# Kernel tuning notes

Measured on AMD Instinct MI355X. Metric: run time of the kernel, lower is better.

## Reference

```python
import jax, jax.numpy as jnp
import numpy as np

N_NODES = 50000
N_EDGES = 100000
NODE_DIM = 6
EDGE_DIM = 4
H = 64        # hidden_dim
HEADS = 4
T = 3         # n_iterations
RED = 16      # CBAM reduction ratio
Z_VALUES = np.array([7.98, 22.98, 38.98, 53.98, 89.98, 180.48], np.float32)


def _ln(x, g, b, eps=1e-5):
    mu = jnp.mean(x, -1, keepdims=True)
    v = jnp.mean((x - mu) ** 2, -1, keepdims=True)
    return (x - mu) * jax.lax.rsqrt(v + eps) * g + b


def _conv1d(x, w, b, pad):
    y = jax.lax.conv_general_dilated(x, w, (1,), [(pad, pad)],
                                     dimension_numbers=('NCH', 'OIH', 'NCH'))
    return y + b[None, :, None]


def _cbam(x, w1, b1, w2, b2, cw1, cb1, cw2, cb2):
    # channel attention: pool over node dim -> [1, 2H] -> MLP -> sigmoid
    cat = jnp.concatenate([x.max(0, keepdims=True), x.mean(0, keepdims=True)], 1)
    cw = jax.nn.sigmoid(jnp.maximum(cat @ w1 + b1, 0.0) @ w2 + b2)  # [1, H]
    x = x * cw
    # spatial attention: pool over feature dim -> conv1d stack over node axis
    sp = jnp.stack([x.max(-1), x.mean(-1)], 0)[None]                # [1, 2, N]
    s = jnp.maximum(_conv1d(sp, cw1, cb1, 2), 0.0)
    s = jax.nn.sigmoid(_conv1d(s, cw2, cb2, 1))                     # [1, 1, N]
    return x * s[0, 0][:, None]


def _forward(x, edge_attr, z_table, W_node, b_node, W_edge, b_edge,
             cn_w1, cn_b1, cn_w2, cn_b2, cn_cw1, cn_cb1, cn_cw2, cn_cb2,
             ce_w1, ce_b1, ce_w2, ce_b2, ce_cw1, ce_cb1, ce_cw2, ce_cb2,
             ln_comb_g, ln_comb_b, Wq, bq, Wk, bk, Wv, bv, Wskip, bskip,
             ln_tc_g, ln_tc_b, Wpn, bpn, Wpe, bpe, Wg, bg,
             Wc1, bc1, Wc2, bc2, edge_index, z_keys):
    n = x.shape[0]
    # bidirectional edges
    src = jnp.concatenate([edge_index[0], edge_index[1]])
    dst = jnp.concatenate([edge_index[1], edge_index[0]])
    eab = jnp.concatenate([edge_attr, edge_attr], 0)
    rel = x[src, :3] - x[dst, :3]

    # z embedding lookup (non-matching z -> index 0, matching torch default)
    zint = jnp.round(x[:, 2]).astype(jnp.int32)
    zidx = jnp.argmax(zint[:, None] == z_keys[None, :], 1)

    nf = jnp.maximum(x @ W_node + b_node, 0.0) + z_table[zidx]
    nf = _cbam(nf, cn_w1, cn_b1, cn_w2, cn_b2, cn_cw1, cn_cb1, cn_cw2, cn_cb2)
    ef = jnp.maximum(jnp.concatenate([eab, rel], 1) @ W_edge + b_edge, 0.0)
    ef = _cbam(ef, ce_w1, ce_b1, ce_w2, ce_b2, ce_cw1, ce_cb1, ce_cw2, ce_cb2)

    scale = float(1.0 / np.sqrt(H))
    for i in range(T):
        x0, e0 = nf, ef
        agg = jax.ops.segment_sum(ef, dst, num_segments=n)
        comb = _ln(jnp.concatenate([nf, agg - nf], 1), ln_comb_g[i], ln_comb_b[i])
        # TransformerConv (PyG): q at dst, k/v at src, segment softmax over dst
        q = (comb @ Wq[i] + bq[i]).reshape(n, HEADS, H)
        k = (comb @ Wk[i] + bk[i]).reshape(n, HEADS, H)
        v = (comb @ Wv[i] + bv[i]).reshape(n, HEADS, H)
        logits = jnp.sum(q[dst] * k[src], -1) * scale           # [2E, HEADS]
        m = jax.ops.segment_max(logits, dst, num_segments=n)
        p = jnp.exp(logits - m[dst])
        denom = jax.ops.segment_sum(p, dst, num_segments=n)
        alpha = p / denom[dst]
        out = jax.ops.segment_sum(alpha[..., None] * v[src], dst, num_segments=n)
        out = out.reshape(n, HEADS * H) + comb @ Wskip[i] + bskip[i]
        out = _ln(out, ln_tc_g[i], ln_tc_b[i])
        npj = out @ Wpn[i] + bpn[i]
        epj = out[src] @ Wpe[i] + bpe[i]
        g = jax.nn.sigmoid(jnp.concatenate([x0, npj], 1) @ Wg[i] + bg[i])
        nf = x0 * g + npj * (1.0 - g)
        g2 = jax.nn.sigmoid(jnp.concatenate([e0, epj], 1) @ Wg[i] + bg[i])
        ef = e0 * g2 + epj * (1.0 - g2)

    s_idx, e_idx = edge_index[0], edge_index[1]
    clf = jnp.concatenate([nf[s_idx], nf[e_idx]], 1)
    return (jnp.maximum(clf @ Wc1 + bc1, 0.0) @ Wc2 + bc2)[:, 0]


def setup_inputs() -> dict:
    key = jax.random.key(0)
    ks = iter(jax.random.split(key, 80))
    def nrm(shape, s=0.05):
        return jax.random.normal(next(ks), shape, jnp.float32) * s
    x = jax.random.normal(next(ks), (N_NODES, NODE_DIM), jnp.float32)
    zch = jax.random.randint(next(ks), (N_NODES,), 0, len(Z_VALUES))
    x = x.at[:, 2].set(jnp.asarray(Z_VALUES)[zch])
    edge_index = jax.random.randint(next(ks), (2, N_EDGES), 0, N_NODES)
    edge_attr = jax.random.normal(next(ks), (N_EDGES, EDGE_DIM), jnp.float32)
    z_keys = jnp.asarray(np.round(Z_VALUES).astype(np.int32))
    HH, r = HEADS * H, H // RED
    def zeros(*s):
        return jnp.zeros(s, jnp.float32)
    inp = dict(
        x=x, edge_attr=edge_attr, edge_index=edge_index, z_keys=z_keys,
        z_table=nrm((len(Z_VALUES), H)),
        W_node=nrm((NODE_DIM, H)), b_node=zeros(H),
        W_edge=nrm((EDGE_DIM + 3, H)), b_edge=zeros(H),
        cn_w1=nrm((2 * H, r)), cn_b1=zeros(r), cn_w2=nrm((r, H)), cn_b2=zeros(H),
        cn_cw1=nrm((1, 2, 5)), cn_cb1=zeros(1), cn_cw2=nrm((1, 1, 3)), cn_cb2=zeros(1),
        ce_w1=nrm((2 * H, r)), ce_b1=zeros(r), ce_w2=nrm((r, H)), ce_b2=zeros(H),
        ce_cw1=nrm((1, 2, 5)), ce_cb1=zeros(1), ce_cw2=nrm((1, 1, 3)), ce_cb2=zeros(1),
        ln_comb_g=jnp.ones((T, 2 * H), jnp.float32), ln_comb_b=zeros(T, 2 * H),
        Wq=nrm((T, 2 * H, HH)), bq=zeros(T, HH),
        Wk=nrm((T, 2 * H, HH)), bk=zeros(T, HH),
        Wv=nrm((T, 2 * H, HH)), bv=zeros(T, HH),
        Wskip=nrm((T, 2 * H, HH)), bskip=zeros(T, HH),
        ln_tc_g=jnp.ones((T, HH), jnp.float32), ln_tc_b=zeros(T, HH),
        Wpn=nrm((T, HH, H)), bpn=zeros(T, H),
        Wpe=nrm((T, HH, H)), bpe=zeros(T, H),
        Wg=nrm((T, 2 * H, H)), bg=zeros(T, H),
        Wc1=nrm((2 * H, H)), bc1=zeros(H), Wc2=nrm((H, 1)), bc2=zeros(1),
    )
    return inp


def reference(x, edge_attr, edge_index, z_keys, z_table, W_node, b_node, W_edge, b_edge,
              cn_w1, cn_b1, cn_w2, cn_b2, cn_cw1, cn_cb1, cn_cw2, cn_cb2,
              ce_w1, ce_b1, ce_w2, ce_b2, ce_cw1, ce_cb1, ce_cw2, ce_cb2,
              ln_comb_g, ln_comb_b, Wq, bq, Wk, bk, Wv, bv, Wskip, bskip,
              ln_tc_g, ln_tc_b, Wpn, bpn, Wpe, bpe, Wg, bg, Wc1, bc1, Wc2, bc2):
    return _forward(x, edge_attr, z_table, W_node, b_node, W_edge, b_edge,
                    cn_w1, cn_b1, cn_w2, cn_b2, cn_cw1, cn_cb1, cn_cw2, cn_cb2,
                    ce_w1, ce_b1, ce_w2, ce_b2, ce_cw1, ce_cb1, ce_cw2, ce_cb2,
                    ln_comb_g, ln_comb_b, Wq, bq, Wk, bk, Wv, bv, Wskip, bskip,
                    ln_tc_g, ln_tc_b, Wpn, bpn, Wpe, bpe, Wg, bg,
                    Wc1, bc1, Wc2, bc2, edge_index, z_keys)
```

## Files before the change

kernel.cpp:

```cpp
#include <hip/hip_runtime.h>


#define LN_EPS 1e-5f
#define PBLK 512

typedef __attribute__((ext_vector_type(8))) short bf16x8;
typedef __attribute__((ext_vector_type(4))) float f32x4;

static __device__ __forceinline__ float wsum(float v) {
#pragma unroll
  for (int d = 32; d > 0; d >>= 1) v += __shfl_xor(v, d);
  return v;
}
static __device__ __forceinline__ float sigm(float x) { return 1.0f / (1.0f + __expf(-x)); }
static __device__ __forceinline__ unsigned short f2bf(float f) {
  unsigned int u = __float_as_uint(f);
  u += 0x7FFFu + ((u >> 16) & 1u);
  return (unsigned short)(u >> 16);
}
static __device__ __forceinline__ float bf2f(unsigned short b) {
  return __uint_as_float(((unsigned int)b) << 16);
}
static __device__ __forceinline__ float4 ld4v(const float* p) { return *(const float4*)p; }
static __device__ __forceinline__ float4 ld4v(const unsigned short* p) {
  union { uint2 u; unsigned short h[4]; } t;
  t.u = *(const uint2*)p;
  return make_float4(bf2f(t.h[0]), bf2f(t.h[1]), bf2f(t.h[2]), bf2f(t.h[3]));
}
static __device__ __forceinline__ void st4v(float* p, float4 v) { *(float4*)p = v; }
static __device__ __forceinline__ void st4v(unsigned short* p, float4 v) {
  union { uint2 u; unsigned short h[4]; } t;
  t.h[0] = f2bf(v.x); t.h[1] = f2bf(v.y); t.h[2] = f2bf(v.z); t.h[3] = f2bf(v.w);
  *(uint2*)p = t.u;
}

__global__ __launch_bounds__(256) void k_zero2(int* __restrict__ a, int* __restrict__ b, int n) {
  int i = blockIdx.x * 256 + threadIdx.x;
  if (i < n) { a[i] = 0; b[i] = 0; }
}

__global__ __launch_bounds__(256) void k_sentinel(float* __restrict__ out, int n) {
  int i = blockIdx.x * 256 + threadIdx.x;
  if (i < n) out[i] = 1.0e6f;
}

__global__ __launch_bounds__(256) void k_hist(const int* __restrict__ ei, int* __restrict__ cnt, int E) {
  int e = blockIdx.x * 256 + threadIdx.x;
  if (e >= 2 * E) return;
  int d = (e < E) ? ei[E + e] : ei[e - E];
  atomicAdd(&cnt[d], 1);
}

__global__ __launch_bounds__(256) void k_scan1(const int* __restrict__ cnt, int* __restrict__ off,
                                               int* __restrict__ bsum, int n) {
  const int t = threadIdx.x;
  const int lane = t & 63, w = t >> 6;
  const int i0 = blockIdx.x * 1024 + t * 4;
  int v0 = (i0 + 0 < n) ? cnt[i0 + 0] : 0;
  int v1 = (i0 + 1 < n) ? cnt[i0 + 1] : 0;
  int v2 = (i0 + 2 < n) ? cnt[i0 + 2] : 0;
  int v3 = (i0 + 3 < n) ? cnt[i0 + 3] : 0;
  int s = v0 + v1 + v2 + v3;
  int sc = s;
#pragma unroll
  for (int d = 1; d < 64; d <<= 1) {
    int tv = __shfl_up(sc, d);
    if (lane >= d) sc += tv;
  }
  __shared__ int wsums[4];
  if (lane == 63) wsums[w] = sc;
  __syncthreads();
  int wbase = 0;
#pragma unroll
  for (int k = 0; k < 4; ++k)
    if (k < w) wbase += wsums[k];
  int run = wbase + sc - s;
  if (i0 + 0 < n) off[i0 + 0] = run; run += v0;
  if (i0 + 1 < n) off[i0 + 1] = run; run += v1;
  if (i0 + 2 < n) off[i0 + 2] = run; run += v2;
  if (i0 + 3 < n) off[i0 + 3] = run;
  if (t == 255) bsum[blockIdx.x] = wbase + sc;
}

__global__ __launch_bounds__(64) void k_scan2(const int* __restrict__ bsum, int* __restrict__ boff,
                                              int* __restrict__ off, int n, int nblk) {
  const int lane = threadIdx.x;
  int carry = 0;
  for (int base = 0; base < nblk; base += 64) {
    int i = base + lane;
    int v = (i < nblk) ? bsum[i] : 0;
    int sc = v;
#pragma unroll
    for (int d = 1; d < 64; d <<= 1) {
      int tv = __shfl_up(sc, d);
      if (lane >= d) sc += tv;
    }
    if (i < nblk) boff[i] = carry + sc - v;
    carry += __shfl(sc, 63);
  }
  if (lane == 0) off[n] = carry;
}

__global__ __launch_bounds__(256) void k_scan3(int* __restrict__ off, const int* __restrict__ boff, int n) {
  int i = blockIdx.x * 256 + threadIdx.x;
  if (i < n) off[i] += boff[i >> 10];
}

__global__ __launch_bounds__(256) void k_scatter(const int* __restrict__ ei, const int* __restrict__ off,
                                                 int* __restrict__ cur, int* __restrict__ elist,
                                                 int* __restrict__ slist, int E) {
  int e = blockIdx.x * 256 + threadIdx.x;
  if (e >= 2 * E) return;
  int d = (e < E) ? ei[E + e] : ei[e - E];
  int pos = atomicAdd(&cur[d], 1);
  int base = off[d] + pos;
  elist[base] = e;
  slist[base] = ei[e];
}

__global__ __launch_bounds__(256) void k_packW(
    const float* __restrict__ Wq, const float* __restrict__ Wk, const float* __restrict__ Wv,
    const float* __restrict__ Ws, const float* __restrict__ bq, const float* __restrict__ bk,
    const float* __restrict__ bv, const float* __restrict__ bs,
    const float* __restrict__ Wpn, const float* __restrict__ Wpe,
    const float* __restrict__ bpn, const float* __restrict__ bpe,
    const float* __restrict__ Wg, const float* __restrict__ Wc1,
    unsigned short* __restrict__ W1t, float* __restrict__ bias1,
    unsigned short* __restrict__ B2t, float* __restrict__ bias2,
    unsigned short* __restrict__ Wg1t, unsigned short* __restrict__ Wc1t) {
  const int S1 = 3 * 1024 * 128, S2 = 3 * 1024, S3 = 3 * 256 * 256, S4 = 3 * 256;
  const int S5 = 3 * 64 * 64, S6 = 2 * 64 * 64;
  int idx = blockIdx.x * 256 + threadIdx.x;
  if (idx < S1) {
    int i = idx / 131072, r = idx % 131072;
    int col = r >> 7, k = r & 127;
    int m = col >> 8, cc = col & 255;
    const float* W = (m == 0) ? Wq : (m == 1) ? Wk : (m == 2) ? Wv : Ws;
    W1t[idx] = f2bf(W[i * 32768 + k * 256 + cc]);
  } else if (idx < S1 + S2) {
    int j = idx - S1;
    int i = j >> 10, col = j & 1023;
    int m = col >> 8, cc = col & 255;
    const float* bsrc = (m == 0) ? bq : (m == 1) ? bk : (m == 2) ? bv : bs;
    bias1[j] = bsrc[i * 256 + cc];
  } else if (idx < S1 + S2 + S3) {
    int j = idx - S1 - S2;
    int i = j / 65536, r = j % 65536;
    int col = r >> 8, k = r & 255;
    float v;
    if (col < 64) v = Wpn[i * 16384 + k * 64 + col];
    else if (col < 128) v = Wpe[i * 16384 + k * 64 + (col - 64)];
    else {
      const float* Wsrc = (col < 192) ? Wpn : Wpe;
      int cc = col & 63;
      float acc = 0.f;
      for (int jj = 0; jj < 64; ++jj)
        acc = fmaf(Wsrc[i * 16384 + k * 64 + jj], Wg[i * 8192 + (64 + jj) * 64 + cc], acc);
      v = acc;
    }
    B2t[j] = f2bf(v);
  } else if (idx < S1 + S2 + S3 + S4) {
    int j = idx - S1 - S2 - S3;
    int i = j >> 8, col = j & 255;
    float v;
    if (col < 64) v = bpn[i * 64 + col];
    else if (col < 128) v = bpe[i * 64 + col - 64];
    else {
      const float* bsrc = (col < 192) ? bpn : bpe;
      int cc = col & 63;
      float acc = 0.f;
      for (int jj = 0; jj < 64; ++jj)
        acc = fmaf(bsrc[i * 64 + jj], Wg[i * 8192 + (64 + jj) * 64 + cc], acc);
      v = acc;
    }
    bias2[j] = v;
  } else if (idx < S1 + S2 + S3 + S4 + S5) {
    int j = idx - S1 - S2 - S3 - S4;
    int i = j / 4096, r = j % 4096;
    int col = r >> 6, k = r & 63;
    Wg1t[j] = f2bf(Wg[i * 8192 + k * 64 + col]);
  } else if (idx < S1 + S2 + S3 + S4 + S5 + S6) {
    int j = idx - S1 - S2 - S3 - S4 - S5;
    int h = j / 4096, r = j % 4096;
    int col = r >> 6, k = r & 63;
    Wc1t[j] = f2bf(Wc1[(h * 64 + k) * 64 + col]);
  }
}

__global__ __launch_bounds__(256) void k_node_embed(
    const float* __restrict__ x, const int* __restrict__ zk, const float* __restrict__ zt,
    const float* __restrict__ Wn, const float* __restrict__ bn, float* __restrict__ nf, int N) {
  int n = blockIdx.x * 4 + (threadIdx.x >> 6);
  int lane = threadIdx.x & 63;
  if (n >= N) return;
  const float* xr = x + (size_t)n * 6;
  float acc = bn[lane];
#pragma unroll
  for (int d = 0; d < 6; ++d) acc = fmaf(xr[d], Wn[d * 64 + lane], acc);
  int zi = __float2int_rn(xr[2]);
  int idx = 0;
#pragma unroll
  for (int t = 5; t >= 0; --t)
    if (zi == zk[t]) idx = t;
  nf[(size_t)n * 64 + lane] = fmaxf(acc, 0.0f) + zt[idx * 64 + lane];
}

__global__ __launch_bounds__(256) void k_edge_embed(
    const float* __restrict__ x, const float* __restrict__ ea, const int* __restrict__ ei,
    const float* __restrict__ We, const float* __restrict__ be,
    unsigned short* __restrict__ ef, int E) {
  int e = blockIdx.x * 4 + (threadIdx.x >> 6);
  int lane = threadIdx.x & 63;
  if (e >= 2 * E) return;
  int e0 = (e < E) ? e : e - E;
  int s = ei[e];
  int d = (e < E) ? ei[E + e] : ei[e - E];
  const float* ar = ea + (size_t)e0 * 4;
  const float* xs = x + (size_t)s * 6;
  const float* xd = x + (size_t)d * 6;
  float in[7];
  in[0] = ar[0]; in[1] = ar[1]; in[2] = ar[2]; in[3] = ar[3];
  in[4] = xs[0] - xd[0]; in[5] = xs[1] - xd[1]; in[6] = xs[2] - xd[2];
  float acc = be[lane];
#pragma unroll
  for (int dd = 0; dd < 7; ++dd) acc = fmaf(in[dd], We[dd * 64 + lane], acc);
  ef[(size_t)e * 64 + lane] = f2bf(fmaxf(acc, 0.0f));
}

template <typename T>
__global__ __launch_bounds__(256) void k_pool_partial(const T* __restrict__ buf, int n,
                                                      float* __restrict__ pm, float* __restrict__ ps) {
  const int w = threadIdx.x >> 6, l = threadIdx.x & 63;
  const int rsub = l >> 4, c4 = (l & 15) << 2;
  float4 mx = make_float4(-INFINITY, -INFINITY, -INFINITY, -INFINITY);
  float4 sm = make_float4(0.f, 0.f, 0.f, 0.f);
  for (int r = blockIdx.x * 16 + w * 4 + rsub; r < n; r += gridDim.x * 16) {
    float4 v = ld4v(buf + (size_t)r * 64 + c4);
    mx.x = fmaxf(mx.x, v.x); mx.y = fmaxf(mx.y, v.y);
    mx.z = fmaxf(mx.z, v.z); mx.w = fmaxf(mx.w, v.w);
    sm.x += v.x; sm.y += v.y; sm.z += v.z; sm.w += v.w;
  }
#pragma unroll
  for (int d = 16; d < 64; d <<= 1) {
    mx.x = fmaxf(mx.x, __shfl_xor(mx.x, d)); mx.y = fmaxf(mx.y, __shfl_xor(mx.y, d));
    mx.z = fmaxf(mx.z, __shfl_xor(mx.z, d)); mx.w = fmaxf(mx.w, __shfl_xor(mx.w, d));
    sm.x += __shfl_xor(sm.x, d); sm.y += __shfl_xor(sm.y, d);
    sm.z += __shfl_xor(sm.z, d); sm.w += __shfl_xor(sm.w, d);
  }
  __shared__ float smx[4][64], ssm[4][64];
  if (l < 16) {
    *(float4*)&smx[w][c4] = mx;
    *(float4*)&ssm[w][c4] = sm;
  }
  __syncthreads();
  if (threadIdx.x < 64) {
    int t = threadIdx.x;
    float m2 = fmaxf(fmaxf(smx[0][t], smx[1][t]), fmaxf(smx[2][t], smx[3][t]));
    float s2 = ssm[0][t] + ssm[1][t] + ssm[2][t] + ssm[3][t];
    pm[blockIdx.x * 64 + t] = m2;
    ps[blockIdx.x * 64 + t] = s2;
  }
}

__global__ __launch_bounds__(256) void k_pool_final(
    const float* __restrict__ pm, const float* __restrict__ ps, int n, int nblk,
    const float* __restrict__ w1, const float* __restrict__ b1,
    const float* __restrict__ w2, const float* __restrict__ b2, float* __restrict__ cw) {
  __shared__ float redm[4][64], reds[4][64];
  __shared__ float cat[128];
  __shared__ float hid[4];
  int t = threadIdx.x;
  int g = t >> 6, col = t & 63;
  float mx = -INFINITY, sm = 0.0f;
  for (int p = g; p < nblk; p += 4) {
    mx = fmaxf(mx, pm[p * 64 + col]);
    sm += ps[p * 64 + col];
  }
  redm[g][col] = mx;
  reds[g][col] = sm;
  __syncthreads();
  if (t < 64) {
    float m2 = fmaxf(fmaxf(redm[0][t], redm[1][t]), fmaxf(redm[2][t], redm[3][t]));
    float s2 = reds[0][t] + reds[1][t] + reds[2][t] + reds[3][t];
    cat[t] = m2;
    cat[64 + t] = s2 / (float)n;
  }
  __syncthreads();
  if (t < 4) {
    float a = b1[t];
    for (int k = 0; k < 128; ++k) a = fmaf(cat[k], w1[k * 4 + t], a);
    hid[t] = fmaxf(a, 0.0f);
  }
  __syncthreads();
  if (t < 64) {
    float a = b2[t];
#pragma unroll
    for (int h = 0; h < 4; ++h) a = fmaf(hid[h], w2[h * 64 + t], a);
    cw[t] = sigm(a);
  }
}

template <typename T>
__global__ __launch_bounds__(256) void k_chan_sp(T* __restrict__ buf, int n,
                                                 const float* __restrict__ cw,
                                                 float* __restrict__ spmax, float* __restrict__ spmean) {
  const int w = threadIdx.x >> 6, l = threadIdx.x & 63;
  const int rsub = l >> 4, c4 = (l & 15) << 2;
  int r = blockIdx.x * 16 + w * 4 + rsub;
  if (r >= n) return;
  float4 cwv = *(const float4*)(cw + c4);
  float4 v = ld4v(buf + (size_t)r * 64 + c4);
  v.x *= cwv.x; v.y *= cwv.y; v.z *= cwv.z; v.w *= cwv.w;
  st4v(buf + (size_t)r * 64 + c4, v);
  float mx = fmaxf(fmaxf(v.x, v.y), fmaxf(v.z, v.w));
  float sm = v.x + v.y + v.z + v.w;
#pragma unroll
  for (int d = 1; d < 16; d <<= 1) {
    mx = fmaxf(mx, __shfl_xor(mx, d));
    sm += __shfl_xor(sm, d);
  }
  if ((l & 15) == 0) {
    spmax[r] = mx;
    spmean[r] = sm * (1.0f / 64.0f);
  }
}

__global__ __launch_bounds__(256) void k_conv(const float* __restrict__ spmax, const float* __restrict__ spmean,
                                              int n, const float* __restrict__ w1, const float* __restrict__ b1,
                                              const float* __restrict__ w2, const float* __restrict__ b2,
                                              float* __restrict__ s) {
  __shared__ float tl[258];
  int base = blockIdx.x * 256;
  for (int q = threadIdx.x; q < 258; q += 256) {
    int p = base - 1 + q;
    float t = 0.0f;
    if (p >= 0 && p < n) {
      float a = b1[0];
#pragma unroll
      for (int h = 0; h < 5; ++h) {
        int pp = p + h - 2;
        if (pp >= 0 && pp < n) a += spmax[pp] * w1[h] + spmean[pp] * w1[5 + h];
      }
      t = fmaxf(a, 0.0f);
    }
    tl[q] = t;
  }
  __syncthreads();
  int o = base + threadIdx.x;
  if (o < n) {
    float a = b2[0] + tl[threadIdx.x] * w2[0] + tl[threadIdx.x + 1] * w2[1] + tl[threadIdx.x + 2] * w2[2];
    s[o] = sigm(a);
  }
}

template <typename T>
__global__ __launch_bounds__(256) void k_row_scale(T* __restrict__ buf, int n, const float* __restrict__ s) {
  int i4 = blockIdx.x * 256 + threadIdx.x;
  if (i4 >= n * 16) return;
  int r = i4 >> 4;
  float sc = s[r];
  float4 v = ld4v(buf + (size_t)i4 * 4);
  v.x *= sc; v.y *= sc; v.z *= sc; v.w *= sc;
  st4v(buf + (size_t)i4 * 4, v);
}

__global__ __launch_bounds__(256) void k_aggcomb(const unsigned short* __restrict__ ef,
                                                 const float* __restrict__ nf,
                                                 const int* __restrict__ off, const int* __restrict__ elist,
                                                 unsigned short* __restrict__ comb, const float* __restrict__ g,
                                                 const float* __restrict__ b, int N) {
  int n = blockIdx.x * 4 + (threadIdx.x >> 6);
  int lane = threadIdx.x & 63;
  if (n >= N) return;
  float agg = 0.0f;
  int i0 = off[n], i1 = off[n + 1];
  for (int idx = i0; idx < i1; ++idx) agg += bf2f(ef[(size_t)elist[idx] * 64 + lane]);
  float y0 = nf[(size_t)n * 64 + lane];
  float y1 = agg - y0;
  float s1 = wsum(y0 + y1);
  float s2 = wsum(y0 * y0 + y1 * y1);
  float mu = s1 * (1.0f / 128.0f);
  float var = s2 * (1.0f / 128.0f) - mu * mu;
  float rs = rsqrtf(fmaxf(var, 0.0f) + LN_EPS);
  comb[(size_t)n * 128 + lane] = f2bf((y0 - mu) * rs * g[lane] + b[lane]);
  comb[(size_t)n * 128 + 64 + lane] = f2bf((y1 - mu) * rs * g[64 + lane] + b[64 + lane]);
}

template <int MODE>
__global__ __launch_bounds__(256) void gemm_mfma(
    const unsigned short* __restrict__ A, int M, int K,
    const unsigned short* __restrict__ Bt, const float* __restrict__ bias,
    unsigned short* __restrict__ outQ, unsigned short* __restrict__ outK,
    unsigned short* __restrict__ outS) {
  __shared__ unsigned short shmem[128 * 136];
  unsigned short* As = shmem;
  unsigned short* Bs = shmem + 128 * 64;
  const int tid = threadIdx.x;
  int bm, bn;
  if (MODE == 0) {
    int cpx = gridDim.x >> 3;
    int wgid = (blockIdx.x & 7) * cpx + (blockIdx.x >> 3);
    bm = (wgid >> 3) * 128;
    bn = (wgid & 7) * 128;
  } else {
    bm = blockIdx.x * 128;
    bn = blockIdx.y * 128;
  }
  const int wid = tid >> 6, lane = tid & 63;
  const int wr = (wid >> 1) * 64, wc = (wid & 1) * 64;
  const int lrow = lane & 15, lkb = (lane >> 4) * 8;
  f32x4 acc[4][4];
#pragma unroll
  for (int m = 0; m < 4; ++m)
#pragma unroll
    for (int n = 0; n < 4; ++n) acc[m][n] = (f32x4){0.f, 0.f, 0.f, 0.f};

  for (int k0 = 0; k0 < K; k0 += 64) {
#pragma unroll
    for (int l = 0; l < 4; ++l) {
      int c = tid + l * 256;
      int row = c >> 3, kc = (c & 7) * 8;
      int sw = row * 64 + (kc ^ ((row & 7) << 3));
      int grow = bm + row;
      bf16x8 v = {0, 0, 0, 0, 0, 0, 0, 0};
      if (grow < M) v = *(const bf16x8*)(A + (size_t)grow * K + k0 + kc);
      *(bf16x8*)&As[sw] = v;
      int gcol = bn + row;
      *(bf16x8*)&Bs[sw] = *(const bf16x8*)(Bt + (size_t)gcol * K + k0 + kc);
    }
    __syncthreads();
#pragma unroll
    for (int ks = 0; ks < 2; ++ks) {
      const int ke = ks * 32 + lkb;
      bf16x8 af[4], bfr[4];
#pragma unroll
      for (int m = 0; m < 4; ++m) {
        int row = wr + m * 16 + lrow;
        af[m] = *(const bf16x8*)&As[row * 64 + (ke ^ ((row & 7) << 3))];
      }
#pragma unroll
      for (int n = 0; n < 4; ++n) {
        int col = wc + n * 16 + lrow;
        bfr[n] = *(const bf16x8*)&Bs[col * 64 + (ke ^ ((col & 7) << 3))];
      }
#pragma unroll
      for (int m = 0; m < 4; ++m)
#pragma unroll
        for (int n = 0; n < 4; ++n)
          acc[m][n] = __builtin_amdgcn_mfma_f32_16x16x32_bf16(af[m], bfr[n], acc[m][n], 0, 0, 0);
    }
    __syncthreads();
  }

  const int colw = lane & 15, rq = (lane >> 4) * 4;
  unsigned short* Cs = shmem;
#pragma unroll
  for (int m = 0; m < 4; ++m) {
#pragma unroll
    for (int n = 0; n < 4; ++n) {
      int col = wc + n * 16 + colw;
      float bv = bias[bn + col];
#pragma unroll
      for (int r = 0; r < 4; ++r) {
        int row = wr + m * 16 + rq + r;
        Cs[row * 136 + col] = f2bf(acc[m][n][r] + bv);
      }
    }
  }
  __syncthreads();
  const int rsub = tid >> 4, c8 = (tid & 15) * 8;
#pragma unroll
  for (int i = 0; i < 8; ++i) {
    int row = i * 16 + rsub;
    int grow = bm + row;
    if (grow >= M) continue;
    uint4 v = *(const uint4*)&Cs[row * 136 + c8];
    if (MODE == 1) {
      *(uint4*)(outQ + (size_t)grow * 256 + bn + c8) = v;
    } else {
      const int proj = bn >> 8;
      int cc = (bn & 255) + c8;
      if (proj == 0) *(uint4*)(outQ + (size_t)grow * 256 + cc) = v;
      else if (proj == 1) *(uint4*)(outK + (size_t)grow * 512 + cc) = v;
      else if (proj == 2) *(uint4*)(outK + (size_t)grow * 512 + 256 + cc) = v;
      else *(uint4*)(outS + (size_t)grow * 256 + cc) = v;
    }
  }
}

template <int UPD>
__global__ __launch_bounds__(256) void gemm_gate(
    const void* __restrict__ Av, int M, const unsigned short* __restrict__ Wt,
    const unsigned short* __restrict__ P, const float* __restrict__ bgv,
    const int* __restrict__ ei, void* __restrict__ updv) {
  __shared__ unsigned short As[128 * 64];
  __shared__ unsigned short Ws[64 * 64];
  const int tid = threadIdx.x;
  const int bm = blockIdx.x * 128;
  if (UPD == 2) {
    const unsigned short* Ab = (const unsigned short*)Av;
#pragma unroll
    for (int l = 0; l < 4; ++l) {
      int u = tid + l * 256;
      int row = u >> 3, kc = (u & 7) * 8;
      int grow = bm + row;
      bf16x8 v = {0, 0, 0, 0, 0, 0, 0, 0};
      if (grow < M) v = *(const bf16x8*)(Ab + (size_t)grow * 64 + kc);
      *(bf16x8*)&As[row * 64 + (kc ^ ((row & 7) << 3))] = v;
    }
  } else {
    const float* Af = (const float*)Av;
#pragma unroll
    for (int l = 0; l < 8; ++l) {
      int u = tid + l * 256;
      int row = u >> 4, k4 = (u & 15) << 2;
      int grow = bm + row;
      float4 v = make_float4(0.f, 0.f, 0.f, 0.f);
      if (grow < M) v = *(const float4*)(Af + (size_t)grow * 64 + k4);
      union { unsigned short h[4]; uint2 q; } pk;
      pk.h[0] = f2bf(v.x); pk.h[1] = f2bf(v.y); pk.h[2] = f2bf(v.z); pk.h[3] = f2bf(v.w);
      *(uint2*)&As[row * 64 + (k4 ^ ((row & 7) << 3))] = pk.q;
    }
  }
#pragma unroll
  for (int l = 0; l < 2; ++l) {
    int u = tid + l * 256;
    int row = u >> 3, kc = (u & 7) * 8;
    *(bf16x8*)&Ws[row * 64 + (kc ^ ((row & 7) << 3))] = *(const bf16x8*)(Wt + row * 64 + kc);
  }
  __syncthreads();
  const int wid = tid >> 6, lane = tid & 63;
  const int wr = wid * 32;
  const int lrow = lane & 15, lkb = (lane >> 4) * 8;
  f32x4 acc[2][4];
#pragma unroll
  for (int m = 0; m < 2; ++m)
#pragma unroll
    for (int n = 0; n < 4; ++n) acc[m][n] = (f32x4){0.f, 0.f, 0.f, 0.f};
#pragma unroll
  for (int ks = 0; ks < 2; ++ks) {
    const int ke = ks * 32 + lkb;
    bf16x8 af[2], wf[4];
#pragma unroll
    for (int m = 0; m < 2; ++m) {
      int row = wr + m * 16 + lrow;
      af[m] = *(const bf16x8*)&As[row * 64 + (ke ^ ((row & 7) << 3))];
    }
#pragma unroll
    for (int n = 0; n < 4; ++n) {
      int col = n * 16 + lrow;
      wf[n] = *(const bf16x8*)&Ws[col * 64 + (ke ^ ((col & 7) << 3))];
    }
#pragma unroll
    for (int m = 0; m < 2; ++m)
#pragma unroll
      for (int n = 0; n < 4; ++n)
        acc[m][n] = __builtin_amdgcn_mfma_f32_16x16x32_bf16(af[m], wf[n], acc[m][n], 0, 0, 0);
  }
  const int colw = lane & 15, rq = (lane >> 4) * 4;
#pragma unroll
  for (int m = 0; m < 2; ++m) {
#pragma unroll
    for (int r = 0; r < 4; ++r) {
      int e = bm + wr + m * 16 + rq + r;
      if (e >= M) continue;
      if (UPD == 0) {
        float* upd = (float*)updv;
#pragma unroll
        for (int n = 0; n < 4; ++n) upd[(size_t)e * 64 + n * 16 + colw] = acc[m][n][r];
      } else if (UPD == 1) {
        float* upd = (float*)updv;
        const unsigned short* Pr = P + (size_t)e * 256;
#pragma unroll
        for (int n = 0; n < 4; ++n) {
          int c = n * 16 + colw;
          float g = sigm(acc[m][n][r] + bf2f(Pr[128 + c]) + bgv[c]);
          size_t oi = (size_t)e * 64 + c;
          upd[oi] = upd[oi] * g + bf2f(Pr[c]) * (1.0f - g);
        }
      } else {
        unsigned short* upd = (unsigned short*)updv;
        int s = ei[e];
        const unsigned short* Pr = P + (size_t)s * 256;
#pragma unroll
        for (int n = 0; n < 4; ++n) {
          int c = n * 16 + colw;
          float g = sigm(acc[m][n][r] + bf2f(Pr[192 + c]) + bgv[c]);
          size_t oi = (size_t)e * 64 + c;
          float vA = bf2f(upd[oi]);
          upd[oi] = f2bf(vA * g + bf2f(Pr[64 + c]) * (1.0f - g));
        }
      }
    }
  }
}

__global__ __launch_bounds__(256) void k_attn(const unsigned short* __restrict__ qo,
                                              const unsigned short* __restrict__ kv,
                                              const unsigned short* __restrict__ skipb, const int* __restrict__ off,
                                              const int* __restrict__ slist,
                                              unsigned short* __restrict__ aob,
                                              const float* __restrict__ g, const float* __restrict__ b, int N) {
  int n = blockIdx.x * 4 + (threadIdx.x >> 6);
  int lane = threadIdx.x & 63;
  if (n >= N) return;
  union { uint2 u; unsigned short h[4]; } qq;
  qq.u = *(const uint2*)(qo + (size_t)n * 256 + 4 * lane);
  float q0 = bf2f(qq.h[0]), q1 = bf2f(qq.h[1]), q2 = bf2f(qq.h[2]), q3 = bf2f(qq.h[3]);
  float m = -INFINITY, lsum = 0.f;
  float a0 = 0.f, a1 = 0.f, a2 = 0.f, a3 = 0.f;
  int i0 = off[n], i1 = off[n + 1];
  int idx = i0;
  for (; idx + 2 <= i1; idx += 2) {
    int sA = slist[idx], sB = slist[idx + 1];
    const unsigned short* kbA = kv + (size_t)sA * 512;
    const unsigned short* kbB = kv + (size_t)sB * 512;
    union { uint2 u; unsigned short h[4]; } kkA, vvA, kkB, vvB;
    kkA.u = *(const uint2*)(kbA + 4 * lane);
    vvA.u = *(const uint2*)(kbA + 256 + 4 * lane);
    kkB.u = *(const uint2*)(kbB + 4 * lane);
    vvB.u = *(const uint2*)(kbB + 256 + 4 * lane);
    float dA = q0 * bf2f(kkA.h[0]) + q1 * bf2f(kkA.h[1]) + q2 * bf2f(kkA.h[2]) + q3 * bf2f(kkA.h[3]);
    float dB = q0 * bf2f(kkB.h[0]) + q1 * bf2f(kkB.h[1]) + q2 * bf2f(kkB.h[2]) + q3 * bf2f(kkB.h[3]);
#pragma unroll
    for (int dd = 1; dd < 16; dd <<= 1) {
      dA += __shfl_xor(dA, dd);
      dB += __shfl_xor(dB, dd);
    }
    dA *= 0.125f;
    dB *= 0.125f;
    float nm, sc, p;
    nm = fmaxf(m, dA); sc = __expf(m - nm); p = __expf(dA - nm);
    lsum = lsum * sc + p;
    a0 = fmaf(p, bf2f(vvA.h[0]), a0 * sc);
    a1 = fmaf(p, bf2f(vvA.h[1]), a1 * sc);
    a2 = fmaf(p, bf2f(vvA.h[2]), a2 * sc);
    a3 = fmaf(p, bf2f(vvA.h[3]), a3 * sc);
    m = nm;
    nm = fmaxf(m, dB); sc = __expf(m - nm); p = __expf(dB - nm);
    lsum = lsum * sc + p;
    a0 = fmaf(p, bf2f(vvB.h[0]), a0 * sc);
    a1 = fmaf(p, bf2f(vvB.h[1]), a1 * sc);
    a2 = fmaf(p, bf2f(vvB.h[2]), a2 * sc);
    a3 = fmaf(p, bf2f(vvB.h[3]), a3 * sc);
    m = nm;
  }
  if (idx < i1) {
    int s = slist[idx];
    const unsigned short* kb = kv + (size_t)s * 512;
    union { uint2 u; unsigned short h[4]; } kk, vv;
    kk.u = *(const uint2*)(kb + 4 * lane);
    vv.u = *(const uint2*)(kb + 256 + 4 * lane);
    float d = q0 * bf2f(kk.h[0]) + q1 * bf2f(kk.h[1]) + q2 * bf2f(kk.h[2]) + q3 * bf2f(kk.h[3]);
#pragma unroll
    for (int dd = 1; dd < 16; dd <<= 1) d += __shfl_xor(d, dd);
    d *= 0.125f;
    float nm = fmaxf(m, d);
    float sc = __expf(m - nm);
    float p = __expf(d - nm);
    lsum = lsum * sc + p;
    a0 = fmaf(p, bf2f(vv.h[0]), a0 * sc);
    a1 = fmaf(p, bf2f(vv.h[1]), a1 * sc);
    a2 = fmaf(p, bf2f(vv.h[2]), a2 * sc);
    a3 = fmaf(p, bf2f(vv.h[3]), a3 * sc);
    m = nm;
  }
  union { uint2 u; unsigned short h[4]; } sb;
  sb.u = *(const uint2*)(skipb + (size_t)n * 256 + 4 * lane);
  float inv = (lsum > 0.f) ? 1.0f / lsum : 0.f;
  float v0 = bf2f(sb.h[0]) + a0 * inv;
  float v1 = bf2f(sb.h[1]) + a1 * inv;
  float v2 = bf2f(sb.h[2]) + a2 * inv;
  float v3 = bf2f(sb.h[3]) + a3 * inv;
  float s1 = wsum(v0 + v1 + v2 + v3);
  float s2 = wsum(v0 * v0 + v1 * v1 + v2 * v2 + v3 * v3);
  float mu = s1 * (1.0f / 256.0f);
  float var = s2 * (1.0f / 256.0f) - mu * mu;
  float rs = rsqrtf(fmaxf(var, 0.0f) + LN_EPS);
  float4 g4 = *(const float4*)(g + 4 * lane);
  float4 b4 = *(const float4*)(b + 4 * lane);
  union { uint2 u; unsigned short h[4]; } ob;
  ob.h[0] = f2bf((v0 - mu) * rs * g4.x + b4.x);
  ob.h[1] = f2bf((v1 - mu) * rs * g4.y + b4.y);
  ob.h[2] = f2bf((v2 - mu) * rs * g4.z + b4.z);
  ob.h[3] = f2bf((v3 - mu) * rs * g4.w + b4.w);
  *(uint2*)(aob + (size_t)n * 256 + 4 * lane) = ob.u;
}

__global__ __launch_bounds__(256) void k_clf_pair(const float* __restrict__ ABt, const float* __restrict__ ABb,
                                                  const int* __restrict__ ei, const float* __restrict__ bc1,
                                                  const float* __restrict__ Wc2, const float* __restrict__ bc2,
                                                  float* __restrict__ out, int E) {
  int e = blockIdx.x * 4 + (threadIdx.x >> 6);
  int lane = threadIdx.x & 63;
  if (e >= E) return;
  int s = ei[e], t = ei[E + e];
  float h = fmaxf(ABt[(size_t)s * 64 + lane] + ABb[(size_t)t * 64 + lane] + bc1[lane], 0.0f);
  float r = wsum(h * Wc2[lane]);
  if (lane == 0) out[e] = r + bc2[0];
}

extern "C" void kernel_launch(void* const* d_in, const int* in_sizes, int n_in,
                              void* d_out, int out_size, void* d_ws, size_t ws_size,
                              hipStream_t stream) {
  const float* x = (const float*)d_in[0];
  const float* edge_attr = (const float*)d_in[1];
  const int* ei = (const int*)d_in[2];
  const int* zk = (const int*)d_in[3];
  const float* z_table = (const float*)d_in[4];
  const float* W_node = (const float*)d_in[5];
  const float* b_node = (const float*)d_in[6];
  const float* W_edge = (const float*)d_in[7];
  const float* b_edge = (const float*)d_in[8];
  const float* cn_w1 = (const float*)d_in[9];
  const float* cn_b1 = (const float*)d_in[10];
  const float* cn_w2 = (const float*)d_in[11];
  const float* cn_b2 = (const float*)d_in[12];
  const float* cn_cw1 = (const float*)d_in[13];
  const float* cn_cb1 = (const float*)d_in[14];
  const float* cn_cw2 = (const float*)d_in[15];
  const float* cn_cb2 = (const float*)d_in[16];
  const float* ce_w1 = (const float*)d_in[17];
  const float* ce_b1 = (const float*)d_in[18];
  const float* ce_w2 = (const float*)d_in[19];
  const float* ce_b2 = (const float*)d_in[20];
  const float* ce_cw1 = (const float*)d_in[21];
  const float* ce_cb1 = (const float*)d_in[22];
  const float* ce_cw2 = (const float*)d_in[23];
  const float* ce_cb2 = (const float*)d_in[24];
  const float* ln_comb_g = (const float*)d_in[25];
  const float* ln_comb_b = (const float*)d_in[26];
  const float* Wq = (const float*)d_in[27];
  const float* bq = (const float*)d_in[28];
  const float* Wk = (const float*)d_in[29];
  const float* bk = (const float*)d_in[30];
  const float* Wv = (const float*)d_in[31];
  const float* bv = (const float*)d_in[32];
  const float* Wskip = (const float*)d_in[33];
  const float* bskip = (const float*)d_in[34];
  const float* ln_tc_g = (const float*)d_in[35];
  const float* ln_tc_b = (const float*)d_in[36];
  const float* Wpn = (const float*)d_in[37];
  const float* bpn = (const float*)d_in[38];
  const float* Wpe = (const float*)d_in[39];
  const float* bpe = (const float*)d_in[40];
  const float* Wg = (const float*)d_in[41];
  const float* bg = (const float*)d_in[42];
  const float* Wc1 = (const float*)d_in[43];
  const float* bc1 = (const float*)d_in[44];
  const float* Wc2 = (const float*)d_in[45];
  const float* bc2 = (const float*)d_in[46];
  float* out = (float*)d_out;

  const int N = in_sizes[0] / 6;
  const int E = in_sizes[2] / 2;
  const int E2 = 2 * E;

  char* p = (char*)d_ws;
  auto carve = [&](size_t bytes) -> void* {
    void* r = (void*)p;
    p += (bytes + 255) & ~(size_t)255;
    return r;
  };
  unsigned short* qo = (unsigned short*)carve((size_t)N * 256 * 2);
  unsigned short* skipb = (unsigned short*)carve((size_t)N * 256 * 2);
  unsigned short* kvb = (unsigned short*)carve((size_t)N * 512 * 2);
  unsigned short* aob = (unsigned short*)carve((size_t)N * 256 * 2);
  unsigned short* efb = (unsigned short*)carve((size_t)E2 * 64 * 2);
  float* nf = (float*)carve((size_t)N * 64 * 4);
  unsigned short* comb = (unsigned short*)carve((size_t)N * 128 * 2);
  unsigned short* W1t = (unsigned short*)carve((size_t)3 * 1024 * 128 * 2);
  float* bias1 = (float*)carve((size_t)3 * 1024 * 4);
  unsigned short* B2t = (unsigned short*)carve((size_t)3 * 256 * 256 * 2);
  float* bias2 = (float*)carve((size_t)3 * 256 * 4);
  unsigned short* Wg1t = (unsigned short*)carve((size_t)3 * 64 * 64 * 2);
  unsigned short* Wc1t = (unsigned short*)carve((size_t)2 * 64 * 64 * 2);
  int* cnt = (int*)carve((size_t)N * 4);
  int* cur = (int*)carve((size_t)N * 4);
  int* off = (int*)carve((size_t)(N + 1) * 4);
  int* elist = (int*)carve((size_t)E2 * 4);
  int* slist = (int*)carve((size_t)E2 * 4);
  int* bsum = (int*)carve((size_t)256 * 4);
  int* boff = (int*)carve((size_t)256 * 4);
  float* pm = (float*)carve((size_t)PBLK * 64 * 4);
  float* ps = (float*)carve((size_t)PBLK * 64 * 4);
  float* cwv = (float*)carve(64 * 4);
  float* spmax = (float*)carve((size_t)E2 * 4);
  float* spmean = (float*)carve((size_t)E2 * 4);
  float* sconv = (float*)carve((size_t)E2 * 4);
  size_t need = (size_t)(p - (char*)d_ws);

  unsigned short* Pb = skipb;
  float* ABt = (float*)aob;
  float* ABb = (float*)aob + (size_t)N * 64;

  auto cdiv = [](int a, int b) { return (a + b - 1) / b; };

  if (ws_size < need) {
    k_sentinel<<<cdiv(E, 256), 256, 0, stream>>>(out, E);
    return;
  }

  k_zero2<<<cdiv(N, 256), 256, 0, stream>>>(cnt, cur, N);
  k_hist<<<cdiv(E2, 256), 256, 0, stream>>>(ei, cnt, E);
  const int nblk = cdiv(N, 1024);
  k_scan1<<<nblk, 256, 0, stream>>>(cnt, off, bsum, N);
  k_scan2<<<1, 64, 0, stream>>>(bsum, boff, off, N, nblk);
  k_scan3<<<cdiv(N, 256), 256, 0, stream>>>(off, boff, N);
  k_scatter<<<cdiv(E2, 256), 256, 0, stream>>>(ei, off, cur, elist, slist, E);

  const int PACK = 3 * 1024 * 128 + 3 * 1024 + 3 * 256 * 256 + 3 * 256 + 3 * 64 * 64 + 2 * 64 * 64;
  k_packW<<<cdiv(PACK, 256), 256, 0, stream>>>(Wq, Wk, Wv, Wskip, bq, bk, bv, bskip,
                                               Wpn, Wpe, bpn, bpe, Wg, Wc1,
                                               W1t, bias1, B2t, bias2, Wg1t, Wc1t);

  k_node_embed<<<cdiv(N, 4), 256, 0, stream>>>(x, zk, z_table, W_node, b_node, nf, N);
  k_edge_embed<<<cdiv(E2, 4), 256, 0, stream>>>(x, edge_attr, ei, W_edge, b_edge, efb, E);

  k_pool_partial<float><<<PBLK, 256, 0, stream>>>(nf, N, pm, ps);
  k_pool_final<<<1, 256, 0, stream>>>(pm, ps, N, PBLK, cn_w1, cn_b1, cn_w2, cn_b2, cwv);
  k_chan_sp<float><<<cdiv(N, 16), 256, 0, stream>>>(nf, N, cwv, spmax, spmean);
  k_conv<<<cdiv(N, 256), 256, 0, stream>>>(spmax, spmean, N, cn_cw1, cn_cb1, cn_cw2, cn_cb2, sconv);
  k_row_scale<float><<<cdiv(N * 16, 256), 256, 0, stream>>>(nf, N, sconv);

  k_pool_partial<unsigned short><<<PBLK, 256, 0, stream>>>(efb, E2, pm, ps);
  k_pool_final<<<1, 256, 0, stream>>>(pm, ps, E2, PBLK, ce_w1, ce_b1, ce_w2, ce_b2, cwv);
  k_chan_sp<unsigned short><<<cdiv(E2, 16), 256, 0, stream>>>(efb, E2, cwv, spmax, spmean);
  k_conv<<<cdiv(E2, 256), 256, 0, stream>>>(spmax, spmean, E2, ce_cw1, ce_cb1, ce_cw2, ce_cb2, sconv);
  k_row_scale<unsigned short><<<cdiv(E2 * 16, 256), 256, 0, stream>>>(efb, E2, sconv);

  const int gqkvs = cdiv(N, 128) * 8;
  dim3 gp(cdiv(N, 128), 2);
  for (int i = 0; i < 3; ++i) {
    k_aggcomb<<<cdiv(N, 4), 256, 0, stream>>>(efb, nf, off, elist, comb,
                                              ln_comb_g + (size_t)i * 128, ln_comb_b + (size_t)i * 128, N);
    gemm_mfma<0><<<gqkvs, 256, 0, stream>>>(comb, N, 128, W1t + (size_t)i * 131072,
                                            bias1 + (size_t)i * 1024, qo, kvb, skipb);
    k_attn<<<cdiv(N, 4), 256, 0, stream>>>(qo, kvb, skipb, off, slist, aob,
                                           ln_tc_g + (size_t)i * 256, ln_tc_b + (size_t)i * 256, N);
    gemm_mfma<1><<<gp, 256, 0, stream>>>(aob, N, 256, B2t + (size_t)i * 65536,
                                         bias2 + (size_t)i * 256, Pb, nullptr, nullptr);
    gemm_gate<1><<<cdiv(N, 128), 256, 0, stream>>>(nf, N, Wg1t + (size_t)i * 4096, Pb,
                                                   bg + (size_t)i * 64, nullptr, nf);
    gemm_gate<2><<<cdiv(E2, 128), 256, 0, stream>>>(efb, E2, Wg1t + (size_t)i * 4096, Pb,
                                                    bg + (size_t)i * 64, ei, efb);
  }

  gemm_gate<0><<<cdiv(N, 128), 256, 0, stream>>>(nf, N, Wc1t, nullptr, nullptr, nullptr, ABt);
  gemm_gate<0><<<cdiv(N, 128), 256, 0, stream>>>(nf, N, Wc1t + 4096, nullptr, nullptr, nullptr, ABb);
  k_clf_pair<<<cdiv(E, 4), 256, 0, stream>>>(ABt, ABb, ei, bc1, Wc2, bc2, out, E);
  (void)out_size;
  (void)n_in;
}
```

Measured before the change: 744.3 us.

## Store edge features in destination-sorted CSR order and unroll attention loop by four

The CBAM row-scale pass now writes edge features into a new buffer permuted into CSR (destination-sorted) order using an inverse permutation computed during scatter. Per-node aggregation therefore reads contiguous rows instead of gathering through an edge list, and the edge gate update indexes the source node via slist in permuted order. The attention kernel also processes four neighbors per iteration to raise memory-level parallelism. The cost is an extra edge-feature buffer and a scattered write during the scaling pass.

```diff
diff --git a/kernel.cpp b/kernel.cpp
--- a/kernel.cpp
+++ b/kernel.cpp
@@ -107,14 +107,14 @@
 }
 
 __global__ __launch_bounds__(256) void k_scatter(const int* __restrict__ ei, const int* __restrict__ off,
-                                                 int* __restrict__ cur, int* __restrict__ elist,
+                                                 int* __restrict__ cur, int* __restrict__ pinv,
                                                  int* __restrict__ slist, int E) {
   int e = blockIdx.x * 256 + threadIdx.x;
   if (e >= 2 * E) return;
   int d = (e < E) ? ei[E + e] : ei[e - E];
   int pos = atomicAdd(&cur[d], 1);
   int base = off[d] + pos;
-  elist[base] = e;
+  pinv[e] = base;
   slist[base] = ei[e];
 }
 
@@ -353,8 +353,7 @@
   }
 }
 
-template <typename T>
-__global__ __launch_bounds__(256) void k_row_scale(T* __restrict__ buf, int n, const float* __restrict__ s) {
+__global__ __launch_bounds__(256) void k_row_scale(float* __restrict__ buf, int n, const float* __restrict__ s) {
   int i4 = blockIdx.x * 256 + threadIdx.x;
   if (i4 >= n * 16) return;
   int r = i4 >> 4;
@@ -364,9 +363,22 @@
   st4v(buf + (size_t)i4 * 4, v);
 }
 
-__global__ __launch_bounds__(256) void k_aggcomb(const unsigned short* __restrict__ ef,
+__global__ __launch_bounds__(256) void k_row_scale_perm(const unsigned short* __restrict__ src, int n,
+                                                        const float* __restrict__ s,
+                                                        const int* __restrict__ pinv,
+                                                        unsigned short* __restrict__ dst) {
+  int i4 = blockIdx.x * 256 + threadIdx.x;
+  if (i4 >= n * 16) return;
+  int r = i4 >> 4, c4 = (i4 & 15) * 4;
+  float sc = s[r];
+  float4 v = ld4v(src + (size_t)r * 64 + c4);
+  v.x *= sc; v.y *= sc; v.z *= sc; v.w *= sc;
+  st4v(dst + (size_t)pinv[r] * 64 + c4, v);
+}
+
+__global__ __launch_bounds__(256) void k_aggcomb(const unsigned short* __restrict__ efc,
                                                  const float* __restrict__ nf,
-                                                 const int* __restrict__ off, const int* __restrict__ elist,
+                                                 const int* __restrict__ off,
                                                  unsigned short* __restrict__ comb, const float* __restrict__ g,
                                                  const float* __restrict__ b, int N) {
   int n = blockIdx.x * 4 + (threadIdx.x >> 6);
@@ -374,7 +386,7 @@
   if (n >= N) return;
   float agg = 0.0f;
   int i0 = off[n], i1 = off[n + 1];
-  for (int idx = i0; idx < i1; ++idx) agg += bf2f(ef[(size_t)elist[idx] * 64 + lane]);
+  for (int idx = i0; idx < i1; ++idx) agg += bf2f(efc[(size_t)idx * 64 + lane]);
   float y0 = nf[(size_t)n * 64 + lane];
   float y1 = agg - y0;
   float s1 = wsum(y0 + y1);
@@ -492,7 +504,7 @@
 __global__ __launch_bounds__(256) void gemm_gate(
     const void* __restrict__ Av, int M, const unsigned short* __restrict__ Wt,
     const unsigned short* __restrict__ P, const float* __restrict__ bgv,
-    const int* __restrict__ ei, void* __restrict__ updv) {
+    const int* __restrict__ srcl, void* __restrict__ updv) {
   __shared__ unsigned short As[128 * 64];
   __shared__ unsigned short Ws[64 * 64];
   const int tid = threadIdx.x;
@@ -580,7 +592,7 @@
         }
       } else {
         unsigned short* upd = (unsigned short*)updv;
-        int s = ei[e];
+        int s = srcl[e];
         const unsigned short* Pr = P + (size_t)s * 256;
 #pragma unroll
         for (int n = 0; n < 4; ++n) {
@@ -611,15 +623,58 @@
   float a0 = 0.f, a1 = 0.f, a2 = 0.f, a3 = 0.f;
   int i0 = off[n], i1 = off[n + 1];
   int idx = i0;
+  for (; idx + 4 <= i1; idx += 4) {
+    int s0 = slist[idx], s1 = slist[idx + 1], s2 = slist[idx + 2], s3 = slist[idx + 3];
+    const unsigned short* kb0 = kv + (size_t)s0 * 512;
+    const unsigned short* kb1 = kv + (size_t)s1 * 512;
+    const unsigned short* kb2 = kv + (size_t)s2 * 512;
+    const unsigned short* kb3 = kv + (size_t)s3 * 512;
+    union { uint2 u; unsigned short h[4]; } kk0, vv0, kk1, vv1, kk2, vv2, kk3, vv3;
+    kk0.u = *(const uint2*)(kb0 + 4 * lane); vv0.u = *(const uint2*)(kb0 + 256 + 4 * lane);
+    kk1.u = *(const uint2*)(kb1 + 4 * lane); vv1.u = *(const uint2*)(kb1 + 256 + 4 * lane);
+    kk2.u = *(const uint2*)(kb2 + 4 * lane); vv2.u = *(const uint2*)(kb2 + 256 + 4 * lane);
+    kk3.u = *(const uint2*)(kb3 + 4 * lane); vv3.u = *(const uint2*)(kb3 + 256 + 4 * lane);
+    float d0 = q0 * bf2f(kk0.h[0]) + q1 * bf2f(kk0.h[1]) + q2 * bf2f(kk0.h[2]) + q3 * bf2f(kk0.h[3]);
+    float d1 = q0 * bf2f(kk1.h[0]) + q1 * bf2f(kk1.h[1]) + q2 * bf2f(kk1.h[2]) + q3 * bf2f(kk1.h[3]);
+    float d2 = q0 * bf2f(kk2.h[0]) + q1 * bf2f(kk2.h[1]) + q2 * bf2f(kk2.h[2]) + q3 * bf2f(kk2.h[3]);
+    float d3 = q0 * bf2f(kk3.h[0]) + q1 * bf2f(kk3.h[1]) + q2 * bf2f(kk3.h[2]) + q3 * bf2f(kk3.h[3]);
+#pragma unroll
+    for (int dd = 1; dd < 16; dd <<= 1) {
+      d0 += __shfl_xor(d0, dd);
+      d1 += __shfl_xor(d1, dd);
+      d2 += __shfl_xor(d2, dd);
+      d3 += __shfl_xor(d3, dd);
+    }
+    d0 *= 0.125f; d1 *= 0.125f; d2 *= 0.125f; d3 *= 0.125f;
+    float nm, sc, p;
+    nm = fmaxf(m, d0); sc = __expf(m - nm); p = __expf(d0 - nm);
+    lsum = lsum * sc + p;
+    a0 = fmaf(p, bf2f(vv0.h[0]), a0 * sc); a1 = fmaf(p, bf2f(vv0.h[1]), a1 * sc);
+    a2 = fmaf(p, bf2f(vv0.h[2]), a2 * sc); a3 = fmaf(p, bf2f(vv0.h[3]), a3 * sc);
+    m = nm;
+    nm = fmaxf(m, d1); sc = __expf(m - nm); p = __expf(d1 - nm);
+    lsum = lsum * sc + p;
+    a0 = fmaf(p, bf2f(vv1.h[0]), a0 * sc); a1 = fmaf(p, bf2f(vv1.h[1]), a1 * sc);
+    a2 = fmaf(p, bf2f(vv1.h[2]), a2 * sc); a3 = fmaf(p, bf2f(vv1.h[3]), a3 * sc);
+    m = nm;
+    nm = fmaxf(m, d2); sc = __expf(m - nm); p = __expf(d2 - nm);
+    lsum = lsum * sc + p;
+    a0 = fmaf(p, bf2f(vv2.h[0]), a0 * sc); a1 = fmaf(p, bf2f(vv2.h[1]), a1 * sc);
+    a2 = fmaf(p, bf2f(vv2.h[2]), a2 * sc); a3 = fmaf(p, bf2f(vv2.h[3]), a3 * sc);
+    m = nm;
+    nm = fmaxf(m, d3); sc = __expf(m - nm); p = __expf(d3 - nm);
+    lsum = lsum * sc + p;
+    a0 = fmaf(p, bf2f(vv3.h[0]), a0 * sc); a1 = fmaf(p, bf2f(vv3.h[1]), a1 * sc);
+    a2 = fmaf(p, bf2f(vv3.h[2]), a2 * sc); a3 = fmaf(p, bf2f(vv3.h[3]), a3 * sc);
+    m = nm;
+  }
   for (; idx + 2 <= i1; idx += 2) {
     int sA = slist[idx], sB = slist[idx + 1];
     const unsigned short* kbA = kv + (size_t)sA * 512;
     const unsigned short* kbB = kv + (size_t)sB * 512;
     union { uint2 u; unsigned short h[4]; } kkA, vvA, kkB, vvB;
-    kkA.u = *(const uint2*)(kbA + 4 * lane);
-    vvA.u = *(const uint2*)(kbA + 256 + 4 * lane);
-    kkB.u = *(const uint2*)(kbB + 4 * lane);
-    vvB.u = *(const uint2*)(kbB + 256 + 4 * lane);
+    kkA.u = *(const uint2*)(kbA + 4 * lane); vvA.u = *(const uint2*)(kbA + 256 + 4 * lane);
+    kkB.u = *(const uint2*)(kbB + 4 * lane); vvB.u = *(const uint2*)(kbB + 256 + 4 * lane);
     float dA = q0 * bf2f(kkA.h[0]) + q1 * bf2f(kkA.h[1]) + q2 * bf2f(kkA.h[2]) + q3 * bf2f(kkA.h[3]);
     float dB = q0 * bf2f(kkB.h[0]) + q1 * bf2f(kkB.h[1]) + q2 * bf2f(kkB.h[2]) + q3 * bf2f(kkB.h[3]);
 #pragma unroll
@@ -627,22 +682,17 @@
       dA += __shfl_xor(dA, dd);
       dB += __shfl_xor(dB, dd);
     }
-    dA *= 0.125f;
-    dB *= 0.125f;
+    dA *= 0.125f; dB *= 0.125f;
     float nm, sc, p;
     nm = fmaxf(m, dA); sc = __expf(m - nm); p = __expf(dA - nm);
     lsum = lsum * sc + p;
-    a0 = fmaf(p, bf2f(vvA.h[0]), a0 * sc);
-    a1 = fmaf(p, bf2f(vvA.h[1]), a1 * sc);
-    a2 = fmaf(p, bf2f(vvA.h[2]), a2 * sc);
-    a3 = fmaf(p, bf2f(vvA.h[3]), a3 * sc);
+    a0 = fmaf(p, bf2f(vvA.h[0]), a0 * sc); a1 = fmaf(p, bf2f(vvA.h[1]), a1 * sc);
+    a2 = fmaf(p, bf2f(vvA.h[2]), a2 * sc); a3 = fmaf(p, bf2f(vvA.h[3]), a3 * sc);
     m = nm;
     nm = fmaxf(m, dB); sc = __expf(m - nm); p = __expf(dB - nm);
     lsum = lsum * sc + p;
-    a0 = fmaf(p, bf2f(vvB.h[0]), a0 * sc);
-    a1 = fmaf(p, bf2f(vvB.h[1]), a1 * sc);
-    a2 = fmaf(p, bf2f(vvB.h[2]), a2 * sc);
-    a3 = fmaf(p, bf2f(vvB.h[3]), a3 * sc);
+    a0 = fmaf(p, bf2f(vvB.h[0]), a0 * sc); a1 = fmaf(p, bf2f(vvB.h[1]), a1 * sc);
+    a2 = fmaf(p, bf2f(vvB.h[2]), a2 * sc); a3 = fmaf(p, bf2f(vvB.h[3]), a3 * sc);
     m = nm;
   }
   if (idx < i1) {
@@ -767,6 +817,7 @@
   unsigned short* kvb = (unsigned short*)carve((size_t)N * 512 * 2);
   unsigned short* aob = (unsigned short*)carve((size_t)N * 256 * 2);
   unsigned short* efb = (unsigned short*)carve((size_t)E2 * 64 * 2);
+  unsigned short* efc = (unsigned short*)carve((size_t)E2 * 64 * 2);
   float* nf = (float*)carve((size_t)N * 64 * 4);
   unsigned short* comb = (unsigned short*)carve((size_t)N * 128 * 2);
   unsigned short* W1t = (unsigned short*)carve((size_t)3 * 1024 * 128 * 2);
@@ -778,7 +829,7 @@
   int* cnt = (int*)carve((size_t)N * 4);
   int* cur = (int*)carve((size_t)N * 4);
   int* off = (int*)carve((size_t)(N + 1) * 4);
-  int* elist = (int*)carve((size_t)E2 * 4);
+  int* pinv = (int*)carve((size_t)E2 * 4);
   int* slist = (int*)carve((size_t)E2 * 4);
   int* bsum = (int*)carve((size_t)256 * 4);
   int* boff = (int*)carve((size_t)256 * 4);
@@ -807,7 +858,7 @@
   k_scan1<<<nblk, 256, 0, stream>>>(cnt, off, bsum, N);
   k_scan2<<<1, 64, 0, stream>>>(bsum, boff, off, N, nblk);
   k_scan3<<<cdiv(N, 256), 256, 0, stream>>>(off, boff, N);
-  k_scatter<<<cdiv(E2, 256), 256, 0, stream>>>(ei, off, cur, elist, slist, E);
+  k_scatter<<<cdiv(E2, 256), 256, 0, stream>>>(ei, off, cur, pinv, slist, E);
 
   const int PACK = 3 * 1024 * 128 + 3 * 1024 + 3 * 256 * 256 + 3 * 256 + 3 * 64 * 64 + 2 * 64 * 64;
   k_packW<<<cdiv(PACK, 256), 256, 0, stream>>>(Wq, Wk, Wv, Wskip, bq, bk, bv, bskip,
@@ -821,18 +872,18 @@
   k_pool_final<<<1, 256, 0, stream>>>(pm, ps, N, PBLK, cn_w1, cn_b1, cn_w2, cn_b2, cwv);
   k_chan_sp<float><<<cdiv(N, 16), 256, 0, stream>>>(nf, N, cwv, spmax, spmean);
   k_conv<<<cdiv(N, 256), 256, 0, stream>>>(spmax, spmean, N, cn_cw1, cn_cb1, cn_cw2, cn_cb2, sconv);
-  k_row_scale<float><<<cdiv(N * 16, 256), 256, 0, stream>>>(nf, N, sconv);
+  k_row_scale<<<cdiv(N * 16, 256), 256, 0, stream>>>(nf, N, sconv);
 
   k_pool_partial<unsigned short><<<PBLK, 256, 0, stream>>>(efb, E2, pm, ps);
   k_pool_final<<<1, 256, 0, stream>>>(pm, ps, E2, PBLK, ce_w1, ce_b1, ce_w2, ce_b2, cwv);
   k_chan_sp<unsigned short><<<cdiv(E2, 16), 256, 0, stream>>>(efb, E2, cwv, spmax, spmean);
   k_conv<<<cdiv(E2, 256), 256, 0, stream>>>(spmax, spmean, E2, ce_cw1, ce_cb1, ce_cw2, ce_cb2, sconv);
-  k_row_scale<unsigned short><<<cdiv(E2 * 16, 256), 256, 0, stream>>>(efb, E2, sconv);
+  k_row_scale_perm<<<cdiv(E2 * 16, 256), 256, 0, stream>>>(efb, E2, sconv, pinv, efc);
 
   const int gqkvs = cdiv(N, 128) * 8;
   dim3 gp(cdiv(N, 128), 2);
   for (int i = 0; i < 3; ++i) {
-    k_aggcomb<<<cdiv(N, 4), 256, 0, stream>>>(efb, nf, off, elist, comb,
+    k_aggcomb<<<cdiv(N, 4), 256, 0, stream>>>(efc, nf, off, comb,
                                               ln_comb_g + (size_t)i * 128, ln_comb_b + (size_t)i * 128, N);
     gemm_mfma<0><<<gqkvs, 256, 0, stream>>>(comb, N, 128, W1t + (size_t)i * 131072,
                                             bias1 + (size_t)i * 1024, qo, kvb, skipb);
@@ -842,8 +893,8 @@
                                          bias2 + (size_t)i * 256, Pb, nullptr, nullptr);
     gemm_gate<1><<<cdiv(N, 128), 256, 0, stream>>>(nf, N, Wg1t + (size_t)i * 4096, Pb,
                                                    bg + (size_t)i * 64, nullptr, nf);
-    gemm_gate<2><<<cdiv(E2, 128), 256, 0, stream>>>(efb, E2, Wg1t + (size_t)i * 4096, Pb,
-                                                    bg + (size_t)i * 64, ei, efb);
+    gemm_gate<2><<<cdiv(E2, 128), 256, 0, stream>>>(efc, E2, Wg1t + (size_t)i * 4096, Pb,
+                                                    bg + (size_t)i * 64, slist, efc);
   }
 
   gemm_gate<0><<<cdiv(N, 128), 256, 0, stream>>>(nf, N, Wc1t, nullptr, nullptr, nullptr, ABt);
```

Measured after the change: 714.7 us. 4.0% less time.
